# Optimization experiments

Hardware: AMD Instinct MI355X
Metric: run time of the kernel (lower is better)

Reference implementation:

```python
import jax, jax.numpy as jnp
import numpy as np

N = 100000       # nodes
E = 3200000      # edges
D_IN = 4
BIG = 32
HID = 2
D_OUT = 4


def setup_inputs() -> dict:
    key = jax.random.key(0)
    ks = jax.random.split(key, 18)
    rn = lambda k, shape, s=0.1: (jax.random.normal(k, shape, jnp.float32) * s)
    inp = {
        "x": jax.random.normal(ks[0], (N, D_IN), jnp.float32),
        "edge_index": jax.random.randint(ks[1], (2, E), 0, N, jnp.int32),
        "eps": jax.random.normal(ks[2], (N, HID), jnp.float32),
        # encoder EdgeConv MLP: Linear(2*D_IN, BIG) -> ReLU -> Linear(BIG, BIG) -> ReLU
        "enc_W1": rn(ks[3], (2 * D_IN, BIG)), "enc_b1": rn(ks[4], (BIG,)),
        "enc_W2": rn(ks[5], (BIG, BIG)),     "enc_b2": rn(ks[6], (BIG,)),
        # mu / logvar heads
        "mu_W": rn(ks[7], (BIG, HID)),  "mu_b": rn(ks[8], (HID,)),
        "var_W": rn(ks[9], (BIG, HID)), "var_b": rn(ks[10], (HID,)),
        # decoder EdgeConv MLP: Linear(2*HID, BIG) -> ReLU -> Linear(BIG, BIG) -> ReLU -> Linear(BIG, D_OUT)
        "dec_W1": rn(ks[11], (2 * HID, BIG)), "dec_b1": rn(ks[12], (BIG,)),
        "dec_W2": rn(ks[13], (BIG, BIG)),     "dec_b2": rn(ks[14], (BIG,)),
        "dec_W3": rn(ks[15], (BIG, D_OUT)),   "dec_b3": rn(ks[16], (D_OUT,)),
    }
    return inp


def _edge_conv_mean(x, src, dst, mlp):
    # PyG EdgeConv: message = nn(concat(x_i, x_j - x_i)) with i=target, j=source,
    # then mean-aggregate messages at each target node.
    xi = x[dst]                      # [E, d]
    xj = x[src]                      # [E, d]
    msg = mlp(jnp.concatenate([xi, xj - xi], axis=-1))   # [E, big]
    s = jax.ops.segment_sum(msg, dst, num_segments=N)    # [N, big]
    cnt = jax.ops.segment_sum(jnp.ones((msg.shape[0], 1), msg.dtype), dst, num_segments=N)
    return s / jnp.maximum(cnt, 1.0)


def reference(x, edge_index, eps,
              enc_W1, enc_b1, enc_W2, enc_b2,
              mu_W, mu_b, var_W, var_b,
              dec_W1, dec_b1, dec_W2, dec_b2, dec_W3, dec_b3):
    src, dst = edge_index[0], edge_index[1]

    def enc_mlp(h):
        h = jax.nn.relu(h @ enc_W1 + enc_b1)
        return jax.nn.relu(h @ enc_W2 + enc_b2)

    def dec_mlp(h):
        h = jax.nn.relu(h @ dec_W1 + dec_b1)
        h = jax.nn.relu(h @ dec_W2 + dec_b2)
        return h @ dec_W3 + dec_b3

    h = _edge_conv_mean(x, src, dst, enc_mlp)     # [N, BIG]
    mu = h @ mu_W + mu_b                          # [N, HID]
    log_var = h @ var_W + var_b                   # [N, HID]
    z = mu + eps * jnp.exp(0.5 * log_var)         # reparameterization
    out = _edge_conv_mean(z, src, dst, dec_mlp)   # [N, D_OUT]
    return out, mu, log_var
```

## Files before the change

kernel.cpp:

```cpp
#include <hip/hip_runtime.h>
#include <hip/hip_bf16.h>

#define NN 100000
#define EE 3200000

#define NBKT 196
#define NBH  391
#define NTOT (NBKT*NBH)
#define NSB  38

typedef short bf16x8 __attribute__((ext_vector_type(8)));
typedef float f32x16 __attribute__((ext_vector_type(16)));

#define WS_SD2F  0
#define WS_TMP2  6400000
#define WS_OFFF  12800000
#define WS_H     12900032
#define WS_PARTF 13053440
#define WS_H4F   13053568
#define WS_OUT4F 13453568
#define WS_ZF    13853568
#define WS_PREP  14053568
#define NEED_FAST ((size_t)14056384 * 4)

#define FB_SD2  0
#define FB_OFF  6400000
#define FB_CNT  6500032
#define FB_PART 6600032
#define FB_H4   6600192
#define FB_OUT4 7000192
#define FB_Z    7400192
#define FB_TMP  6600192
#define FB_PREP 7600192

static __device__ __forceinline__ unsigned short f2bf_fast(float f) {
    unsigned u = __builtin_bit_cast(unsigned, f);
    return (unsigned short)((u + 0x7fffu + ((u >> 16) & 1u)) >> 16);
}

static __device__ __forceinline__ unsigned cvtpk(float a, float b) {
    unsigned r;
    asm("v_cvt_pk_bf16_f32 %0, %1, %2" : "=v"(r) : "v"(a), "v"(b));
    return r;
}
static __device__ __forceinline__ void pl32swap(unsigned &a, unsigned &b) {
    asm("v_permlane32_swap_b32 %0, %1" : "+v"(a), "+v"(b));
}

__global__ __launch_bounds__(256) void zero_kernel(int4* __restrict__ p, int n4)
{
    int i = blockIdx.x * 256 + threadIdx.x;
    if (i < n4) p[i] = make_int4(0, 0, 0, 0);
}

__global__ __launch_bounds__(128) void wprep_kernel(
    const float* __restrict__ encW1, const float* __restrict__ encb1,
    const float* __restrict__ encW2,
    const float* __restrict__ muW,   const float* __restrict__ vW,
    const float* __restrict__ decW1, const float* __restrict__ decb1,
    const float* __restrict__ decW2,
    const float* __restrict__ decW3, unsigned int* __restrict__ prep)
{
    int t = threadIdx.x;
    int v = t >> 6, l = t & 63;
    int j = l & 31, h = l >> 5;
    const float* W1 = v ? decW1 : encW1;
    const float* b1 = v ? decb1 : encb1;
    const float* W2 = v ? decW2 : encW2;
    int K1 = v ? 4 : 8;
    unsigned short frag[5][8];
#pragma unroll
    for (int i = 0; i < 8; ++i) {
        unsigned short f0;
        if (h == 0) f0 = (i < K1) ? f2bf_fast(W1[i * 32 + j]) : (unsigned short)0;
        else        f0 = (i == 0) ? f2bf_fast(b1[j]) : (unsigned short)0;
        frag[0][i] = f0;
        int k0 = 8 * h + i, k1 = 16 + 8 * h + i;
        frag[1][i] = f2bf_fast(W2[k0 * 32 + j]);
        frag[2][i] = f2bf_fast(W2[k1 * 32 + j]);
        unsigned short w0 = 0, w1 = 0;
        if (j < 4) {
            if (v == 0) {
                w0 = (j < 2) ? f2bf_fast(muW[k0 * 2 + j]) : f2bf_fast(vW[k0 * 2 + (j - 2)]);
                w1 = (j < 2) ? f2bf_fast(muW[k1 * 2 + j]) : f2bf_fast(vW[k1 * 2 + (j - 2)]);
            } else {
                w0 = f2bf_fast(decW3[k0 * 4 + j]);
                w1 = f2bf_fast(decW3[k1 * 4 + j]);
            }
        }
        frag[3][i] = w0; frag[4][i] = w1;
    }
    uint4* fp = (uint4*)prep;
#pragma unroll
    for (int f = 0; f < 5; ++f) {
        uint4 wds;
        wds.x = (unsigned)frag[f][0] | ((unsigned)frag[f][1] << 16);
        wds.y = (unsigned)frag[f][2] | ((unsigned)frag[f][3] << 16);
        wds.z = (unsigned)frag[f][4] | ((unsigned)frag[f][5] << 16);
        wds.w = (unsigned)frag[f][6] | ((unsigned)frag[f][7] << 16);
        fp[(v * 5 + f) * 64 + l] = wds;
    }
}


__global__ __launch_bounds__(256) void bhist(
    const int* __restrict__ ei, int* __restrict__ H)
{
    __shared__ int hist[NBKT];
    int t = threadIdx.x;
    if (t < NBKT) hist[t] = 0;
    __syncthreads();
    int base = blockIdx.x * 8192;
#pragma unroll
    for (int k = 0; k < 32; ++k) {
        int e = base + k * 256 + t;
        if (e < EE) atomicAdd(&hist[ei[EE + e] >> 9], 1);
    }
    __syncthreads();
    if (t < NBKT) H[t * NBH + blockIdx.x] = hist[t];
}

__global__ __launch_bounds__(256) void spart(
    const int* __restrict__ H, int n, int* __restrict__ part)
{
    int t = threadIdx.x;
    int base = blockIdx.x * 2048 + t * 8;
    int s = 0;
#pragma unroll
    for (int k = 0; k < 8; ++k) { int i = base + k; if (i < n) s += H[i]; }
    __shared__ int red[256];
    red[t] = s;
    __syncthreads();
    for (int d = 128; d > 0; d >>= 1) {
        if (t < d) red[t] += red[t + d];
        __syncthreads();
    }
    if (t == 0) part[blockIdx.x] = red[0];
}

__global__ __launch_bounds__(256) void spscan(int* __restrict__ part, int np)
{
    __shared__ int sa[256], sbuf[256];
    int t = threadIdx.x;
    int v = (t < np) ? part[t] : 0;
    int *pa = sa, *pb = sbuf;
    pa[t] = v;
    __syncthreads();
    for (int d = 1; d < 256; d <<= 1) {
        pb[t] = pa[t] + ((t >= d) ? pa[t - d] : 0);
        __syncthreads();
        int* tp = pa; pa = pb; pb = tp;
    }
    if (t < np) part[t] = pa[t] - v;
}

__global__ __launch_bounds__(256) void sfinal(
    int* __restrict__ H, int n, const int* __restrict__ part)
{
    int t = threadIdx.x;
    int base = blockIdx.x * 2048 + t * 8;
    int v[8]; int s = 0;
#pragma unroll
    for (int k = 0; k < 8; ++k) { int i = base + k; v[k] = (i < n) ? H[i] : 0; s += v[k]; }
    __shared__ int sa[256], sbuf[256];
    int *pa = sa, *pb = sbuf;
    pa[t] = s;
    __syncthreads();
    for (int d = 1; d < 256; d <<= 1) {
        pb[t] = pa[t] + ((t >= d) ? pa[t - d] : 0);
        __syncthreads();
        int* tp = pa; pa = pb; pb = tp;
    }
    int run = part[blockIdx.x] + pa[t] - s;
#pragma unroll
    for (int k = 0; k < 8; ++k) { int i = base + k; if (i < n) { H[i] = run; run += v[k]; } }
}

__global__ __launch_bounds__(256) void bscatter(
    const int* __restrict__ ei, const int* __restrict__ S, unsigned* __restrict__ tmp2)
{
    __shared__ int cur[NBKT];
    int t = threadIdx.x;
    if (t < NBKT) cur[t] = S[t * NBH + blockIdx.x];
    __syncthreads();
    int base = blockIdx.x * 8192;
#pragma unroll
    for (int k = 0; k < 32; ++k) {
        int e = base + k * 256 + t;
        if (e < EE) {
            int s = ei[e], d = ei[EE + e];
            int p = atomicAdd(&cur[d >> 9], 1);
            tmp2[p] = ((unsigned)(d & 511) << 17) | (unsigned)s;
        }
    }
}

__global__ __launch_bounds__(1024) void bsort(
    const unsigned* __restrict__ tmp2, const int* __restrict__ S,
    int2* __restrict__ sd2, int* __restrict__ off)
{
    int b = blockIdx.x, t = threadIdx.x;
    int bstart = S[b * NBH];
    int bend = (b < NBKT - 1) ? S[(b + 1) * NBH] : EE;
    __shared__ int hist[512], sa[512], sbuf[512];
    if (t < 512) hist[t] = 0;
    __syncthreads();
    for (int e = bstart + t; e < bend; e += 1024)
        atomicAdd(&hist[(tmp2[e] >> 17) & 511], 1);
    __syncthreads();
    int v = 0;
    if (t < 512) { v = hist[t]; sa[t] = v; }
    __syncthreads();
    int *pa = sa, *pb = sbuf;
    for (int d = 1; d < 512; d <<= 1) {
        if (t < 512) pb[t] = pa[t] + ((t >= d) ? pa[t - d] : 0);
        __syncthreads();
        int* tp = pa; pa = pb; pb = tp;
    }
    if (t < 512) {
        int base = bstart + pa[t] - v;
        int n = b * 512 + t;
        if (n < NN) off[n] = base;
        hist[t] = base;
    }
    if (b == 0 && t == 0) off[NN] = EE;
    __syncthreads();
    for (int e = bstart + t; e < bend; e += 1024) {
        unsigned ed = tmp2[e];
        int bin = (int)((ed >> 17) & 511);
        int p = atomicAdd(&hist[bin], 1);
        sd2[p] = make_int2((int)(ed & 0x1FFFFu), (b << 9) | bin);
    }
}


__global__ __launch_bounds__(256) void rank_kernel(
    const int* __restrict__ ei, int* __restrict__ cnt, unsigned char* __restrict__ tmp)
{
    int e = blockIdx.x * 256 + threadIdx.x;
    int d = ei[EE + e];
    tmp[e] = (unsigned char)atomicAdd(&cnt[d], 1);
}

__global__ __launch_bounds__(256) void partial_kernel(
    const int* __restrict__ cnt, int* __restrict__ partials)
{
    int i0 = blockIdx.x * 1024 + threadIdx.x * 4;
    int s = 0;
    if (i0 + 3 < NN) {
        int4 v = *(const int4*)(cnt + i0);
        s = v.x + v.y + v.z + v.w;
    } else {
        for (int i = i0; i < NN; ++i) s += cnt[i];
    }
#pragma unroll
    for (int d = 1; d < 64; d <<= 1) s += __shfl_xor(s, d);
    __shared__ int ws_[4];
    if ((threadIdx.x & 63) == 0) ws_[threadIdx.x >> 6] = s;
    __syncthreads();
    if (threadIdx.x == 0) partials[blockIdx.x] = ws_[0] + ws_[1] + ws_[2] + ws_[3];
}

__global__ __launch_bounds__(128) void scan_partials(
    int* __restrict__ partials, int* __restrict__ off)
{
    __shared__ int ls[128];
    int t = threadIdx.x;
    int v = (t < 98) ? partials[t] : 0;
    ls[t] = v;
    __syncthreads();
#pragma unroll
    for (int d = 1; d < 128; d <<= 1) {
        int u = (t >= d) ? ls[t - d] : 0;
        __syncthreads();
        ls[t] += u;
        __syncthreads();
    }
    if (t < 98) partials[t] = ls[t] - v;
    if (t == 127) off[NN] = ls[127];
}

__global__ __launch_bounds__(256) void final_scan(
    const int* __restrict__ cnt, const int* __restrict__ partials, int* __restrict__ off)
{
    int t = threadIdx.x;
    int i0 = blockIdx.x * 1024 + t * 4;
    int4 v = {0, 0, 0, 0};
    if (i0 + 3 < NN) {
        v = *(const int4*)(cnt + i0);
    } else {
        int tv[4] = {0, 0, 0, 0};
        for (int k = 0; k < 4 && i0 + k < NN; ++k) tv[k] = cnt[i0 + k];
        v.x = tv[0]; v.y = tv[1]; v.z = tv[2]; v.w = tv[3];
    }
    int s = v.x + v.y + v.z + v.w;
    __shared__ int ls[256];
    ls[t] = s;
    __syncthreads();
#pragma unroll
    for (int d = 1; d < 256; d <<= 1) {
        int u = (t >= d) ? ls[t - d] : 0;
        __syncthreads();
        ls[t] += u;
        __syncthreads();
    }
    int base = partials[blockIdx.x] + ls[t] - s;
    int4 o;
    o.x = base; o.y = base + v.x; o.z = o.y + v.y; o.w = o.z + v.z;
    if (i0 + 3 < NN) {
        *(int4*)(off + i0) = o;
    } else {
        int oo[4] = {o.x, o.y, o.z, o.w};
        for (int k = 0; k < 4 && i0 + k < NN; ++k) off[i0 + k] = oo[k];
    }
}

__global__ __launch_bounds__(256) void place_kernel(
    const int* __restrict__ ei, const int* __restrict__ off,
    const unsigned char* __restrict__ tmp, int2* __restrict__ sd2)
{
    int e = blockIdx.x * 256 + threadIdx.x;
    int s = ei[e], d = ei[EE + e];
    int p = off[d] + (int)tmp[e];
    sd2[p] = make_int2(s, d);
}

__global__ __launch_bounds__(256, 4) void edge_mfma(
    const float* __restrict__ feat, int fdim,
    const uint4* __restrict__ wfrag, const float* __restrict__ b2,
    const int2* __restrict__ sd2,
    float* __restrict__ agg4)
{
    __shared__ int   sd[4][128];
    __shared__ float sm4[4][128][5];
    int t = threadIdx.x;
    int w = t >> 6, l = t & 63;
    int h = l >> 5;
    int ebase = (blockIdx.x * 4 + w) * 128;

    bf16x8 A1  = __builtin_bit_cast(bf16x8, wfrag[l]);
    bf16x8 A2a = __builtin_bit_cast(bf16x8, wfrag[64 + l]);
    bf16x8 A2b = __builtin_bit_cast(bf16x8, wfrag[128 + l]);
    bf16x8 A3a = __builtin_bit_cast(bf16x8, wfrag[192 + l]);
    bf16x8 A3b = __builtin_bit_cast(bf16x8, wfrag[256 + l]);

    f32x16 cb;
    {
        float4 q0 = *(const float4*)(b2 + 4 * h);
        float4 q1 = *(const float4*)(b2 + 8 + 4 * h);
        float4 q2 = *(const float4*)(b2 + 16 + 4 * h);
        float4 q3 = *(const float4*)(b2 + 24 + 4 * h);
        cb[0] = q0.x; cb[1] = q0.y; cb[2] = q0.z; cb[3] = q0.w;
        cb[4] = q1.x; cb[5] = q1.y; cb[6] = q1.z; cb[7] = q1.w;
        cb[8] = q2.x; cb[9] = q2.y; cb[10] = q2.z; cb[11] = q2.w;
        cb[12] = q3.x; cb[13] = q3.y; cb[14] = q3.z; cb[15] = q3.w;
    }

    f32x16 czero = {0.f,0.f,0.f,0.f,0.f,0.f,0.f,0.f,0.f,0.f,0.f,0.f,0.f,0.f,0.f,0.f};

    auto tile = [&](const f32x16& D1, float& o0, float& o1, float& o2, float& o3) {
        unsigned c0 = cvtpk(fmaxf(D1[0], 0.f),  fmaxf(D1[1], 0.f));
        unsigned c1 = cvtpk(fmaxf(D1[2], 0.f),  fmaxf(D1[3], 0.f));
        unsigned c2 = cvtpk(fmaxf(D1[4], 0.f),  fmaxf(D1[5], 0.f));
        unsigned c3 = cvtpk(fmaxf(D1[6], 0.f),  fmaxf(D1[7], 0.f));
        unsigned c4 = cvtpk(fmaxf(D1[8], 0.f),  fmaxf(D1[9], 0.f));
        unsigned c5 = cvtpk(fmaxf(D1[10], 0.f), fmaxf(D1[11], 0.f));
        unsigned c6 = cvtpk(fmaxf(D1[12], 0.f), fmaxf(D1[13], 0.f));
        unsigned c7 = cvtpk(fmaxf(D1[14], 0.f), fmaxf(D1[15], 0.f));
        pl32swap(c0, c2); pl32swap(c1, c3); pl32swap(c4, c6); pl32swap(c5, c7);
        bf16x8 B2a = __builtin_bit_cast(bf16x8, make_uint4(c0, c1, c2, c3));
        bf16x8 B2b = __builtin_bit_cast(bf16x8, make_uint4(c4, c5, c6, c7));
        f32x16 acc = cb;
        acc = __builtin_amdgcn_mfma_f32_32x32x16_bf16(A2a, B2a, acc, 0, 0, 0);
        acc = __builtin_amdgcn_mfma_f32_32x32x16_bf16(A2b, B2b, acc, 0, 0, 0);
        unsigned d0 = cvtpk(fmaxf(acc[0], 0.f),  fmaxf(acc[1], 0.f));
        unsigned d1 = cvtpk(fmaxf(acc[2], 0.f),  fmaxf(acc[3], 0.f));
        unsigned d2 = cvtpk(fmaxf(acc[4], 0.f),  fmaxf(acc[5], 0.f));
        unsigned d3 = cvtpk(fmaxf(acc[6], 0.f),  fmaxf(acc[7], 0.f));
        unsigned d4 = cvtpk(fmaxf(acc[8], 0.f),  fmaxf(acc[9], 0.f));
        unsigned d5 = cvtpk(fmaxf(acc[10], 0.f), fmaxf(acc[11], 0.f));
        unsigned d6 = cvtpk(fmaxf(acc[12], 0.f), fmaxf(acc[13], 0.f));
        unsigned d7 = cvtpk(fmaxf(acc[14], 0.f), fmaxf(acc[15], 0.f));
        pl32swap(d0, d2); pl32swap(d1, d3); pl32swap(d4, d6); pl32swap(d5, d7);
        bf16x8 B3a = __builtin_bit_cast(bf16x8, make_uint4(d0, d1, d2, d3));
        bf16x8 B3b = __builtin_bit_cast(bf16x8, make_uint4(d4, d5, d6, d7));
        f32x16 D3 = czero;
        D3 = __builtin_amdgcn_mfma_f32_32x32x16_bf16(A3a, B3a, D3, 0, 0, 0);
        D3 = __builtin_amdgcn_mfma_f32_32x32x16_bf16(A3b, B3b, D3, 0, 0, 0);
        o0 = D3[0]; o1 = D3[1]; o2 = D3[2]; o3 = D3[3];
    };

#pragma unroll
    for (int p = 0; p < 2; ++p) {
        int eb = ebase + 64 * p;
        int2 me = sd2[eb + l];
        sd[w][64 * p + l] = me.y;

        unsigned F0 = 0, F1 = 0, F2 = 0, F3 = 0;
        if (fdim == 4) {
            float4 xd = *(const float4*)(feat + 4 * me.y);
            float4 xs = *(const float4*)(feat + 4 * me.x);
            F0 = cvtpk(xd.x, xd.y);
            F1 = cvtpk(xd.z, xd.w);
            F2 = cvtpk(xs.x - xd.x, xs.y - xd.y);
            F3 = cvtpk(xs.z - xd.z, xs.w - xd.w);
        } else {
            float2 zd = *(const float2*)(feat + 2 * me.y);
            float2 zs = *(const float2*)(feat + 2 * me.x);
            F0 = cvtpk(zd.x, zd.y);
            F1 = cvtpk(zs.x - zd.x, zs.y - zd.y);
        }
        unsigned G0 = 0x00003F80u, G1 = 0, G2 = 0, G3 = 0;
        pl32swap(F0, G0);
        pl32swap(F1, G1);
        pl32swap(F2, G2);
        pl32swap(F3, G3);
        bf16x8 B1a = __builtin_bit_cast(bf16x8, make_uint4(F0, F1, F2, F3));
        bf16x8 B1b = __builtin_bit_cast(bf16x8, make_uint4(G0, G1, G2, G3));

        float o0, o1, o2, o3;
        f32x16 D1a = __builtin_amdgcn_mfma_f32_32x32x16_bf16(A1, B1a, czero, 0, 0, 0);
        tile(D1a, o0, o1, o2, o3);
        if (h == 0) {
            sm4[w][64 * p + l][0] = o0; sm4[w][64 * p + l][1] = o1;
            sm4[w][64 * p + l][2] = o2; sm4[w][64 * p + l][3] = o3;
        }
        f32x16 D1b = __builtin_amdgcn_mfma_f32_32x32x16_bf16(A1, B1b, czero, 0, 0, 0);
        tile(D1b, o0, o1, o2, o3);
        if (h == 0) {
            sm4[w][64 * p + 32 + l][0] = o0; sm4[w][64 * p + 32 + l][1] = o1;
            sm4[w][64 * p + 32 + l][2] = o2; sm4[w][64 * p + 32 + l][3] = o3;
        }
    }

    asm volatile("" ::: "memory");

    int c = l & 3, e0 = (l >> 2) * 8;
    int cur = sd[w][e0];
    float acc4 = 0.f;
#pragma unroll
    for (int k = 0; k < 8; ++k) {
        int dr = sd[w][e0 + k];
        if (dr != cur) { atomicAdd(&agg4[cur * 4 + c], acc4); acc4 = 0.f; cur = dr; }
        acc4 += sm4[w][e0 + k][c];
    }
    atomicAdd(&agg4[cur * 4 + c], acc4);
}

__global__ __launch_bounds__(256) void node_kernel(
    const float* __restrict__ h4, const int* __restrict__ off,
    const float* __restrict__ eps,
    const float* __restrict__ mub, const float* __restrict__ vb,
    float* __restrict__ z, float* __restrict__ out)
{
    int n = blockIdx.x * 256 + threadIdx.x;
    if (n >= NN) return;
    float inv = 1.f / fmaxf((float)(off[n + 1] - off[n]), 1.f);
    float4 a = *(const float4*)(h4 + 4 * n);
    float mu0 = a.x * inv + mub[0], mu1 = a.y * inv + mub[1];
    float lv0 = a.z * inv + vb[0],  lv1 = a.w * inv + vb[1];
    out[4 * NN + 2 * n]     = mu0;
    out[4 * NN + 2 * n + 1] = mu1;
    out[6 * NN + 2 * n]     = lv0;
    out[6 * NN + 2 * n + 1] = lv1;
    float2 zz;
    zz.x = mu0 + eps[2 * n]     * expf(0.5f * lv0);
    zz.y = mu1 + eps[2 * n + 1] * expf(0.5f * lv1);
    *(float2*)(z + 2 * n) = zz;
}

__global__ __launch_bounds__(256) void final_kernel(
    const float* __restrict__ o4, const int* __restrict__ off,
    const float* __restrict__ b3, float* __restrict__ out)
{
    int n = blockIdx.x * 256 + threadIdx.x;
    if (n >= NN) return;
    float inv = 1.f / fmaxf((float)(off[n + 1] - off[n]), 1.f);
    float4 a = *(const float4*)(o4 + 4 * n);
    float4 r;
    r.x = a.x * inv + b3[0]; r.y = a.y * inv + b3[1];
    r.z = a.z * inv + b3[2]; r.w = a.w * inv + b3[3];
    *(float4*)(out + 4 * n) = r;
}

extern "C" void kernel_launch(void* const* d_in, const int* in_sizes, int n_in,
                              void* d_out, int out_size, void* d_ws, size_t ws_size,
                              hipStream_t stream)
{
    const float* x     = (const float*)d_in[0];
    const int*   ei    = (const int*)d_in[1];
    const float* eps   = (const float*)d_in[2];
    const float* encW1 = (const float*)d_in[3];
    const float* encb1 = (const float*)d_in[4];
    const float* encW2 = (const float*)d_in[5];
    const float* encb2 = (const float*)d_in[6];
    const float* muW   = (const float*)d_in[7];
    const float* mub   = (const float*)d_in[8];
    const float* vW    = (const float*)d_in[9];
    const float* vb    = (const float*)d_in[10];
    const float* decW1 = (const float*)d_in[11];
    const float* decb1 = (const float*)d_in[12];
    const float* decW2 = (const float*)d_in[13];
    const float* decb2 = (const float*)d_in[14];
    const float* decW3 = (const float*)d_in[15];
    const float* decb3 = (const float*)d_in[16];

    int*   wsI = (int*)d_ws;
    float* wsF = (float*)d_ws;
    dim3 blk(256);
    dim3 egrid(6250);
    dim3 ngrid((NN + 255) / 256);

    int2* sd2; int* off; float* h4; float* out4; float* z; unsigned int* prep;

    if (ws_size >= NEED_FAST) {
        sd2  = (int2*)(wsI + WS_SD2F);
        unsigned* tmp2 = (unsigned*)(wsI + WS_TMP2);
        off  = wsI + WS_OFFF;
        int* H    = wsI + WS_H;
        int* part = wsI + WS_PARTF;
        h4   = wsF + WS_H4F;
        out4 = wsF + WS_OUT4F;
        z    = wsF + WS_ZF;
        prep = (unsigned int*)(wsI + WS_PREP);

        zero_kernel<<<dim3(782), blk, 0, stream>>>((int4*)(wsF + WS_H4F), 200000);
        wprep_kernel<<<dim3(1), dim3(128), 0, stream>>>(
            encW1, encb1, encW2, muW, vW,
            decW1, decb1, decW2, decW3, prep);

        bhist<<<dim3(NBH), blk, 0, stream>>>(ei, H);
        spart<<<dim3(NSB), blk, 0, stream>>>(H, NTOT, part);
        spscan<<<dim3(1), blk, 0, stream>>>(part, NSB);
        sfinal<<<dim3(NSB), blk, 0, stream>>>(H, NTOT, part);
        bscatter<<<dim3(NBH), blk, 0, stream>>>(ei, H, tmp2);
        bsort<<<dim3(NBKT), dim3(1024), 0, stream>>>(tmp2, H, sd2, off);
    } else {
        sd2  = (int2*)(wsI + FB_SD2);
        off  = wsI + FB_OFF;
        int* cnt  = wsI + FB_CNT;
        int* part = wsI + FB_PART;
        unsigned char* tmp = (unsigned char*)(wsI + FB_TMP);
        h4   = wsF + FB_H4;
        out4 = wsF + FB_OUT4;
        z    = wsF + FB_Z;
        prep = (unsigned int*)(wsI + FB_PREP);

        zero_kernel<<<dim3(98), blk, 0, stream>>>((int4*)(wsI + FB_CNT), 25000);
        wprep_kernel<<<dim3(1), dim3(128), 0, stream>>>(
            encW1, encb1, encW2, muW, vW,
            decW1, decb1, decW2, decW3, prep);
        rank_kernel<<<dim3(12500), blk, 0, stream>>>(ei, cnt, tmp);
        partial_kernel<<<dim3(98), blk, 0, stream>>>(cnt, part);
        scan_partials<<<dim3(1), dim3(128), 0, stream>>>(part, off);
        final_scan<<<dim3(98), blk, 0, stream>>>(cnt, part, off);
        place_kernel<<<dim3(12500), blk, 0, stream>>>(ei, off, tmp, sd2);
        zero_kernel<<<dim3(782), blk, 0, stream>>>((int4*)(wsF + FB_H4), 200000);
    }

    const uint4* wf = (const uint4*)prep;

    edge_mfma<<<egrid, blk, 0, stream>>>(x, 4, wf, encb2, sd2, h4);
    node_kernel<<<ngrid, blk, 0, stream>>>(h4, off, eps, mub, vb, z, (float*)d_out);
    edge_mfma<<<egrid, blk, 0, stream>>>(z, 2, wf + 5 * 64, decb2, sd2, out4);
    final_kernel<<<ngrid, blk, 0, stream>>>(out4, off, decb3, (float*)d_out);
}
```

Measured before the change: 151.8 us.

## Fuse zeroing and weight prep into histogram kernel; single-block scan

Folds the buffer-zeroing and weight-fragment preparation into the bucket histogram kernel, and replaces the three-kernel partial/scan/final prefix sum with one 1024-thread block that scans all ~76.6k histogram entries. This removes five kernel launches and their inter-kernel gaps from the fast path. The single-block scan runs serially over 76-element chunks per thread with uncoalesced strided reads, so it may be slower per element than the multi-block version.

```diff
diff --git a/kernel.cpp b/kernel.cpp
--- a/kernel.cpp
+++ b/kernel.cpp
@@ -7,7 +7,6 @@
 #define NBKT 196
 #define NBH  391
 #define NTOT (NBKT*NBH)
-#define NSB  38
 
 typedef short bf16x8 __attribute__((ext_vector_type(8)));
 typedef float f32x16 __attribute__((ext_vector_type(16)));
@@ -103,11 +102,26 @@
 }
 
 
-__global__ __launch_bounds__(256) void bhist(
-    const int* __restrict__ ei, int* __restrict__ H)
+__global__ __launch_bounds__(256) void bhist_fused(
+    const int* __restrict__ ei, int* __restrict__ H,
+    int4* __restrict__ zbuf,
+    const float* __restrict__ encW1, const float* __restrict__ encb1,
+    const float* __restrict__ encW2,
+    const float* __restrict__ muW,   const float* __restrict__ vW,
+    const float* __restrict__ decW1, const float* __restrict__ decb1,
+    const float* __restrict__ decW2,
+    const float* __restrict__ decW3, unsigned int* __restrict__ prep)
 {
     __shared__ int hist[NBKT];
     int t = threadIdx.x;
+
+    {
+        int zi = blockIdx.x * 512 + t;
+        if (zi < 200000) zbuf[zi] = make_int4(0, 0, 0, 0);
+        zi += 256;
+        if (zi < 200000) zbuf[zi] = make_int4(0, 0, 0, 0);
+    }
+
     if (t < NBKT) hist[t] = 0;
     __syncthreads();
     int base = blockIdx.x * 8192;
@@ -118,62 +132,68 @@
     }
     __syncthreads();
     if (t < NBKT) H[t * NBH + blockIdx.x] = hist[t];
-}
-
-__global__ __launch_bounds__(256) void spart(
-    const int* __restrict__ H, int n, int* __restrict__ part)
-{
-    int t = threadIdx.x;
-    int base = blockIdx.x * 2048 + t * 8;
+
+    if (blockIdx.x == 0 && t < 128) {
+        int v = t >> 6, l = t & 63;
+        int j = l & 31, h = l >> 5;
+        const float* W1 = v ? decW1 : encW1;
+        const float* b1 = v ? decb1 : encb1;
+        const float* W2 = v ? decW2 : encW2;
+        int K1 = v ? 4 : 8;
+        unsigned short frag[5][8];
+#pragma unroll
+        for (int i = 0; i < 8; ++i) {
+            unsigned short f0;
+            if (h == 0) f0 = (i < K1) ? f2bf_fast(W1[i * 32 + j]) : (unsigned short)0;
+            else        f0 = (i == 0) ? f2bf_fast(b1[j]) : (unsigned short)0;
+            frag[0][i] = f0;
+            int k0 = 8 * h + i, k1 = 16 + 8 * h + i;
+            frag[1][i] = f2bf_fast(W2[k0 * 32 + j]);
+            frag[2][i] = f2bf_fast(W2[k1 * 32 + j]);
+            unsigned short w0 = 0, w1 = 0;
+            if (j < 4) {
+                if (v == 0) {
+                    w0 = (j < 2) ? f2bf_fast(muW[k0 * 2 + j]) : f2bf_fast(vW[k0 * 2 + (j - 2)]);
+                    w1 = (j < 2) ? f2bf_fast(muW[k1 * 2 + j]) : f2bf_fast(vW[k1 * 2 + (j - 2)]);
+                } else {
+                    w0 = f2bf_fast(decW3[k0 * 4 + j]);
+                    w1 = f2bf_fast(decW3[k1 * 4 + j]);
+                }
+            }
+            frag[3][i] = w0; frag[4][i] = w1;
+        }
+        uint4* fp = (uint4*)prep;
+#pragma unroll
+        for (int f = 0; f < 5; ++f) {
+            uint4 wds;
+            wds.x = (unsigned)frag[f][0] | ((unsigned)frag[f][1] << 16);
+            wds.y = (unsigned)frag[f][2] | ((unsigned)frag[f][3] << 16);
+            wds.z = (unsigned)frag[f][4] | ((unsigned)frag[f][5] << 16);
+            wds.w = (unsigned)frag[f][6] | ((unsigned)frag[f][7] << 16);
+            fp[(v * 5 + f) * 64 + l] = wds;
+        }
+    }
+}
+
+__global__ __launch_bounds__(1024) void scan_all(int* __restrict__ H, int n)
+{
+    const int CH = 76;
+    __shared__ int ls[1024];
+    int t = threadIdx.x;
+    int lo = t * CH;
+    int hi = lo + CH; if (hi > n) hi = n;
     int s = 0;
-#pragma unroll
-    for (int k = 0; k < 8; ++k) { int i = base + k; if (i < n) s += H[i]; }
-    __shared__ int red[256];
-    red[t] = s;
-    __syncthreads();
-    for (int d = 128; d > 0; d >>= 1) {
-        if (t < d) red[t] += red[t + d];
-        __syncthreads();
-    }
-    if (t == 0) part[blockIdx.x] = red[0];
-}
-
-__global__ __launch_bounds__(256) void spscan(int* __restrict__ part, int np)
-{
-    __shared__ int sa[256], sbuf[256];
-    int t = threadIdx.x;
-    int v = (t < np) ? part[t] : 0;
-    int *pa = sa, *pb = sbuf;
-    pa[t] = v;
-    __syncthreads();
-    for (int d = 1; d < 256; d <<= 1) {
-        pb[t] = pa[t] + ((t >= d) ? pa[t - d] : 0);
-        __syncthreads();
-        int* tp = pa; pa = pb; pb = tp;
-    }
-    if (t < np) part[t] = pa[t] - v;
-}
-
-__global__ __launch_bounds__(256) void sfinal(
-    int* __restrict__ H, int n, const int* __restrict__ part)
-{
-    int t = threadIdx.x;
-    int base = blockIdx.x * 2048 + t * 8;
-    int v[8]; int s = 0;
-#pragma unroll
-    for (int k = 0; k < 8; ++k) { int i = base + k; v[k] = (i < n) ? H[i] : 0; s += v[k]; }
-    __shared__ int sa[256], sbuf[256];
-    int *pa = sa, *pb = sbuf;
-    pa[t] = s;
-    __syncthreads();
-    for (int d = 1; d < 256; d <<= 1) {
-        pb[t] = pa[t] + ((t >= d) ? pa[t - d] : 0);
-        __syncthreads();
-        int* tp = pa; pa = pb; pb = tp;
-    }
-    int run = part[blockIdx.x] + pa[t] - s;
-#pragma unroll
-    for (int k = 0; k < 8; ++k) { int i = base + k; if (i < n) { H[i] = run; run += v[k]; } }
+    for (int i = lo; i < hi; ++i) s += H[i];
+    ls[t] = s;
+    __syncthreads();
+    for (int d = 1; d < 1024; d <<= 1) {
+        int u = (t >= d) ? ls[t - d] : 0;
+        __syncthreads();
+        ls[t] += u;
+        __syncthreads();
+    }
+    int run = ls[t] - s;
+    for (int i = lo; i < hi; ++i) { int v = H[i]; H[i] = run; run += v; }
 }
 
 __global__ __launch_bounds__(256) void bscatter(
@@ -518,21 +538,16 @@
         unsigned* tmp2 = (unsigned*)(wsI + WS_TMP2);
         off  = wsI + WS_OFFF;
         int* H    = wsI + WS_H;
-        int* part = wsI + WS_PARTF;
         h4   = wsF + WS_H4F;
         out4 = wsF + WS_OUT4F;
         z    = wsF + WS_ZF;
         prep = (unsigned int*)(wsI + WS_PREP);
 
-        zero_kernel<<<dim3(782), blk, 0, stream>>>((int4*)(wsF + WS_H4F), 200000);
-        wprep_kernel<<<dim3(1), dim3(128), 0, stream>>>(
+        bhist_fused<<<dim3(NBH), blk, 0, stream>>>(
+            ei, H, (int4*)(wsF + WS_H4F),
             encW1, encb1, encW2, muW, vW,
             decW1, decb1, decW2, decW3, prep);
-
-        bhist<<<dim3(NBH), blk, 0, stream>>>(ei, H);
-        spart<<<dim3(NSB), blk, 0, stream>>>(H, NTOT, part);
-        spscan<<<dim3(1), blk, 0, stream>>>(part, NSB);
-        sfinal<<<dim3(NSB), blk, 0, stream>>>(H, NTOT, part);
+        scan_all<<<dim3(1), dim3(1024), 0, stream>>>(H, NTOT);
         bscatter<<<dim3(NBH), blk, 0, stream>>>(ei, H, tmp2);
         bsort<<<dim3(NBKT), dim3(1024), 0, stream>>>(tmp2, H, sd2, off);
     } else {
```

Result: slower. 253.8 us (+67.2%).
